# Kernel tuning notes

Measured on AMD Instinct MI355X. Metric: run time of the kernel, lower is better.

## Reference

```python
import jax, jax.numpy as jnp
import numpy as np


def setup_inputs() -> dict:
    key = jax.random.key(0)
    k0, k1, k2, k3, k4 = jax.random.split(key, 5)
    B, S, H, I, E = 4, 2048, 1024, 3584, 8
    scale = 0.02
    return {
        "hidden_states": jax.random.normal(k0, (B, S, H), jnp.float32),
        "gate_w": jax.random.normal(k1, (E, H), jnp.float32) * scale,
        "Wg": jax.random.normal(k2, (E, I, H), jnp.float32) * scale,
        "Wu": jax.random.normal(k3, (E, I, H), jnp.float32) * scale,
        "Wd": jax.random.normal(k4, (E, H, I), jnp.float32) * scale,
        "top_k": 2,
    }


def reference(hidden_states, gate_w, Wg, Wu, Wd, top_k):
    B, S, H = hidden_states.shape
    E = gate_w.shape[0]
    x = hidden_states.reshape(-1, H)  # [N, H]

    # Router: softmax in float32 (matches torch dtype=torch.float), then top-k + renorm.
    router_logits = x @ gate_w.T  # [N, E]
    routing_probs = jax.nn.softmax(router_logits.astype(jnp.float32), axis=-1)
    top_w, sel = jax.lax.top_k(routing_probs, top_k)  # [N, K]
    top_w = top_w / jnp.sum(top_w, axis=-1, keepdims=True)
    top_w = top_w.astype(x.dtype)

    # Combined per-token weight for each expert: sum of top-k weights routed to it.
    # comb[n, e] = sum_k top_w[n, k] * (sel[n, k] == e)
    comb = jnp.einsum("nk,nke->ne", top_w, jax.nn.one_hot(sel, E, dtype=x.dtype))

    out = jnp.zeros_like(x)
    for e in range(E):  # fixed small loop over experts (structurally distinct weights)
        h = jax.nn.silu(x @ Wg[e].T) * (x @ Wu[e].T)  # [N, I] SwiGLU
        out = out + (h @ Wd[e].T) * comb[:, e:e + 1]
    return out.reshape(B, S, H), router_logits
```

## Files before the change

### kernel.cpp

```cpp
#include <hip/hip_runtime.h>
#include <hip/hip_bf16.h>

#define N_TOK 8192
#define H_DIM 1024
#define I_DIM 3584
#define N_EXP 8
#define N_PAIR (N_TOK * 2)

#define BM 256
#define BN 128
#define BK 32
#define MAX_TILES 72

#define NPAN1 (I_DIM / BN)
#define NPAN2 (H_DIM / BN)
#define NWG1  (MAX_TILES * NPAN1)
#define NWG2  (MAX_TILES * NPAN2 * 2)

typedef short bf16x8 __attribute__((ext_vector_type(8)));
typedef float f32x4 __attribute__((ext_vector_type(4)));

#define CFENCE() asm volatile("" ::: "memory")


#define WS_CNT      0
#define WS_FILL     64
#define WS_OFF      128
#define WS_NTILES   192
#define WS_TILETAB  256
#define WS_SEL      2048
#define WS_WGT      (WS_SEL    + 2 * N_TOK * 4)
#define WS_PTOK     (WS_WGT    + 2 * N_TOK * 4)
#define WS_PW       (WS_PTOK   + N_PAIR * 4)
#define WS_XBF      (WS_PW     + N_PAIR * 4)
#define WS_HBUF     (WS_XBF    + (size_t)N_TOK * H_DIM * 2)
#define WBF_ELEMS   ((size_t)N_EXP * I_DIM * H_DIM)
#define WS_WGBF     (WS_HBUF + (size_t)N_PAIR * I_DIM * 2)
#define WS_WUBF     (WS_WGBF + WBF_ELEMS * 2)
#define WS_END      (WS_WUBF + WBF_ELEMS * 2)

__device__ __forceinline__ unsigned short f2bf(float f) {
  unsigned int u = __float_as_uint(f);
  unsigned int r = (u + 0x7fffu + ((u >> 16) & 1u)) >> 16;
  return (unsigned short)r;
}

__device__ __forceinline__ uint4 pack8(float4 a, float4 b) {
  uint4 r;
  r.x = (unsigned)f2bf(a.x) | ((unsigned)f2bf(a.y) << 16);
  r.y = (unsigned)f2bf(a.z) | ((unsigned)f2bf(a.w) << 16);
  r.z = (unsigned)f2bf(b.x) | ((unsigned)f2bf(b.y) << 16);
  r.w = (unsigned)f2bf(b.z) | ((unsigned)f2bf(b.w) << 16);
  return r;
}

__device__ __forceinline__ void gll16(const ushort* g, ushort* l) {
  __builtin_amdgcn_global_load_lds(
      (const __attribute__((address_space(1))) unsigned int*)g,
      (__attribute__((address_space(3))) unsigned int*)l, 16, 0, 0);
}

__global__ __launch_bounds__(64) void k_router(
    const float* __restrict__ x, const float* __restrict__ gw,
    float* __restrict__ logits, int* __restrict__ sel,
    float* __restrict__ wgt, int* __restrict__ cnt,
    ushort* __restrict__ xbf)
{
  const int n = blockIdx.x;
  const int lane = threadIdx.x;
  const float4* xr = (const float4*)(x + (size_t)n * H_DIM + lane * 16);
  float4 x0 = xr[0], x1 = xr[1], x2 = xr[2], x3 = xr[3];

  uint4* xo = (uint4*)(xbf + (size_t)n * H_DIM + lane * 16);
  xo[0] = pack8(x0, x1);
  xo[1] = pack8(x2, x3);

  float l[N_EXP];
#pragma unroll
  for (int e = 0; e < N_EXP; ++e) {
    const float4* wr = (const float4*)(gw + e * H_DIM + lane * 16);
    float4 w0 = wr[0], w1 = wr[1], w2 = wr[2], w3 = wr[3];
    float p = x0.x * w0.x + x0.y * w0.y + x0.z * w0.z + x0.w * w0.w
            + x1.x * w1.x + x1.y * w1.y + x1.z * w1.z + x1.w * w1.w
            + x2.x * w2.x + x2.y * w2.y + x2.z * w2.z + x2.w * w2.w
            + x3.x * w3.x + x3.y * w3.y + x3.z * w3.z + x3.w * w3.w;
#pragma unroll
    for (int o = 32; o >= 1; o >>= 1) p += __shfl_xor(p, o, 64);
    l[e] = p;
  }
  float m = l[0];
#pragma unroll
  for (int e = 1; e < N_EXP; ++e) m = fmaxf(m, l[e]);
  float pr[N_EXP]; float den = 0.f;
#pragma unroll
  for (int e = 0; e < N_EXP; ++e) { pr[e] = expf(l[e] - m); den += pr[e]; }
#pragma unroll
  for (int e = 0; e < N_EXP; ++e) pr[e] /= den;
  int i0 = 0; float p0 = pr[0];
#pragma unroll
  for (int e = 1; e < N_EXP; ++e) { if (pr[e] > p0) { p0 = pr[e]; i0 = e; } }
  int i1 = -1; float p1 = -1.f;
#pragma unroll
  for (int e = 0; e < N_EXP; ++e) { if (e != i0 && pr[e] > p1) { p1 = pr[e]; i1 = e; } }
  float rs = 1.f / (p0 + p1);
  if (lane == 0) {
    float* lo = logits + (size_t)n * N_EXP;
#pragma unroll
    for (int e = 0; e < N_EXP; ++e) lo[e] = l[e];
    sel[2 * n] = i0; sel[2 * n + 1] = i1;
    wgt[2 * n] = p0 * rs; wgt[2 * n + 1] = p1 * rs;
    atomicAdd(&cnt[i0], 1);
    atomicAdd(&cnt[i1], 1);
  }
}

__global__ void k_prefix(const int* __restrict__ cnt, int* __restrict__ off,
                         int* __restrict__ ntiles, int* __restrict__ tab)
{
  if (threadIdx.x != 0 || blockIdx.x != 0) return;
  int acc = 0, nt = 0;
  for (int e = 0; e < N_EXP; ++e) {
    off[e] = acc;
    int c = cnt[e];
    for (int r = 0; r < c; r += BM) {
      tab[nt * 3 + 0] = e;
      tab[nt * 3 + 1] = acc + r;
      tab[nt * 3 + 2] = (c - r < BM) ? (c - r) : BM;
      nt++;
    }
    acc += c;
  }
  off[N_EXP] = acc;
  *ntiles = nt;
}

__global__ __launch_bounds__(256) void k_scatter(
    const int* __restrict__ sel, const float* __restrict__ wgt,
    const int* __restrict__ off, int* __restrict__ fill,
    int* __restrict__ ptok, float* __restrict__ pw)
{
  int n = blockIdx.x * 256 + threadIdx.x;
  if (n >= N_TOK) return;
#pragma unroll
  for (int k = 0; k < 2; ++k) {
    int e = sel[2 * n + k];
    int pos = atomicAdd(&fill[e], 1);
    int row = off[e] + pos;
    ptok[row] = n;
    pw[row] = wgt[2 * n + k];
  }
}

__global__ __launch_bounds__(256) void k_cvtw(const float* __restrict__ src,
                                              ushort* __restrict__ dst)
{
  size_t i = (size_t)blockIdx.x * 256 + threadIdx.x;
  const float4* s = (const float4*)(src + i * 8);
  float4 a = s[0], b = s[1];
  ((uint4*)dst)[i] = pack8(a, b);
}


__global__ __launch_bounds__(512) void k_mlp1b(
    const ushort* __restrict__ Wg, const ushort* __restrict__ Wu,
    const ushort* __restrict__ xbf, const int* __restrict__ ptok,
    const int* __restrict__ ntiles, const int* __restrict__ tab,
    ushort* __restrict__ hbuf)
{
  __shared__ ushort sA[2][BM * BK];
  __shared__ ushort sG[2][BN * BK];
  __shared__ ushort sU[2][BN * BK];
  __shared__ int stok[BM];

  const int orig = blockIdx.x;
  const int lin = (orig & 7) * (NWG1 >> 3) + (orig >> 3);
  const int tile = lin / NPAN1;
  const int i0 = (lin % NPAN1) * BN;

  if (tile >= *ntiles) return;
  const int e = tab[tile * 3 + 0];
  const int row0 = tab[tile * 3 + 1];
  const int nrows = tab[tile * 3 + 2];
  const int t = threadIdx.x;

  if (t < BM) {
    int tt = t < nrows ? t : (nrows - 1);
    stok[t] = ptok[row0 + tt];
  }
  __syncthreads();

  const int ak = (((t & 3) ^ ((t >> 3) & 3)) * 8);
  const int ar = t >> 2;
  const ushort* ga0 = xbf + (size_t)stok[ar] * H_DIM + ak;
  const ushort* ga1 = xbf + (size_t)stok[128 + ar] * H_DIM + ak;

  const ushort* gg0 = Wg + (size_t)e * I_DIM * H_DIM + (size_t)(i0 + ar) * H_DIM + ak;
  const ushort* gu0 = Wu + (size_t)e * I_DIM * H_DIM + (size_t)(i0 + ar) * H_DIM + ak;

  const int lane = t & 63, wid = t >> 6;
  const int wm = wid >> 1, wn = wid & 1;
  const int fr = lane & 15, fq = lane >> 4;
  const int fs = (fq ^ ((fr >> 1) & 3)) * 8;

  f32x4 ag[4][4], au[4][4];
#pragma unroll
  for (int m = 0; m < 4; ++m)
#pragma unroll
    for (int n = 0; n < 4; ++n) { ag[m][n] = (f32x4){0,0,0,0}; au[m][n] = (f32x4){0,0,0,0}; }

#define STAGE1(b, kt) do {                      \
    gll16(ga0 + (kt), &sA[b][t * 8]);           \
    gll16(ga1 + (kt), &sA[b][(512 + t) * 8]);   \
    gll16(gg0 + (kt), &sG[b][t * 8]);           \
    gll16(gu0 + (kt), &sU[b][t * 8]);           \
  } while (0)

#define COMPUTE1(b) do {                                                     \
    bf16x8 a[4], bg[4], bu[4];                                               \
    _Pragma("unroll")                                                        \
    for (int m = 0; m < 4; ++m)                                              \
      a[m] = *(const bf16x8*)(&sA[b][(wm * 64 + m * 16 + fr) * BK + fs]);    \
    _Pragma("unroll")                                                        \
    for (int n = 0; n < 4; ++n) {                                            \
      bg[n] = *(const bf16x8*)(&sG[b][(wn * 64 + n * 16 + fr) * BK + fs]);   \
      bu[n] = *(const bf16x8*)(&sU[b][(wn * 64 + n * 16 + fr) * BK + fs]);   \
    }                                                                        \
    _Pragma("unroll")                                                        \
    for (int m = 0; m < 4; ++m)                                              \
      _Pragma("unroll")                                                      \
      for (int n = 0; n < 4; ++n) {                                          \
        ag[m][n] = __builtin_amdgcn_mfma_f32_16x16x32_bf16(a[m], bg[n], ag[m][n], 0, 0, 0); \
        au[m][n] = __builtin_amdgcn_mfma_f32_16x16x32_bf16(a[m], bu[n], au[m][n], 0, 0, 0); \
      }                                                                      \
  } while (0)

  const int NK = H_DIM / BK;
  STAGE1(0, 0);
  CFENCE();
  STAGE1(1, BK);
#pragma unroll 2
  for (int ki = 0; ki < NK - 2; ++ki) {
    const int cur = ki & 1;
    asm volatile("s_waitcnt vmcnt(4)" ::: "memory");
    __builtin_amdgcn_s_barrier();
    CFENCE();
    __builtin_amdgcn_sched_barrier(0);
    COMPUTE1(cur);
    asm volatile("s_waitcnt lgkmcnt(0)" ::: "memory");
    __builtin_amdgcn_sched_barrier(0);
    __builtin_amdgcn_s_barrier();
    CFENCE();
    STAGE1(cur, (ki + 2) * BK);
  }
  asm volatile("s_waitcnt vmcnt(4)" ::: "memory");
  __builtin_amdgcn_s_barrier();
  CFENCE();
  __builtin_amdgcn_sched_barrier(0);
  COMPUTE1(0);
  CFENCE();
  asm volatile("s_waitcnt vmcnt(0) lgkmcnt(0)" ::: "memory");
  __builtin_amdgcn_s_barrier();
  CFENCE();
  __builtin_amdgcn_sched_barrier(0);
  COMPUTE1(1);
#undef STAGE1
#undef COMPUTE1

#pragma unroll
  for (int m = 0; m < 4; ++m) {
    const int rb = wm * 64 + m * 16 + fq * 4;
#pragma unroll
    for (int n = 0; n < 4; ++n) {
      const int col = i0 + wn * 64 + n * 16 + fr;
#pragma unroll
      for (int r = 0; r < 4; ++r) {
        const int row = rb + r;
        if (row < nrows) {
          float g = ag[m][n][r], u = au[m][n][r];
          float hv = (g / (1.f + __expf(-g))) * u;
          hbuf[(size_t)(row0 + row) * I_DIM + col] = f2bf(hv);
        }
      }
    }
  }
}

__global__ __launch_bounds__(512) void k_mlp2b(
    const ushort* __restrict__ Wd, const ushort* __restrict__ hbuf,
    const int* __restrict__ ptok, const float* __restrict__ pw,
    const int* __restrict__ ntiles, const int* __restrict__ tab,
    float* __restrict__ out)
{
  __shared__ ushort sA[2][BM * BK];
  __shared__ ushort sB[2][BN * BK];
  __shared__ int stok[BM];
  __shared__ float sw[BM];

  const int orig = blockIdx.x;
  const int lin = (orig & 7) * (NWG2 >> 3) + (orig >> 3);
  const int tile = lin >> 4;
  const int rem = lin & 15;
  const int j0 = (rem >> 1) * BN;
  const int kz = rem & 1;

  if (tile >= *ntiles) return;
  const int e = tab[tile * 3 + 0];
  const int row0 = tab[tile * 3 + 1];
  const int nrows = tab[tile * 3 + 2];
  const int t = threadIdx.x;

  if (t < BM) {
    int tt = t < nrows ? t : (nrows - 1);
    stok[t] = ptok[row0 + tt];
    sw[t] = pw[row0 + tt];
  }
  __syncthreads();

  const int KHALF = I_DIM / 2;
  const int kbase = kz * KHALF;

  const int ak = (((t & 3) ^ ((t >> 3) & 3)) * 8);
  const int ar = t >> 2;
  int arow0 = row0 + ar;        if (arow0 > N_PAIR - 1) arow0 = N_PAIR - 1;
  int arow1 = row0 + 128 + ar;  if (arow1 > N_PAIR - 1) arow1 = N_PAIR - 1;
  const ushort* ga0 = hbuf + (size_t)arow0 * I_DIM + kbase + ak;
  const ushort* ga1 = hbuf + (size_t)arow1 * I_DIM + kbase + ak;

  const ushort* gb0 = Wd + (size_t)e * H_DIM * I_DIM + (size_t)(j0 + ar) * I_DIM + kbase + ak;

  const int lane = t & 63, wid = t >> 6;
  const int wm = wid >> 1, wn = wid & 1;
  const int fr = lane & 15, fq = lane >> 4;
  const int fs = (fq ^ ((fr >> 1) & 3)) * 8;

  f32x4 ac[4][4];
#pragma unroll
  for (int m = 0; m < 4; ++m)
#pragma unroll
    for (int n = 0; n < 4; ++n) ac[m][n] = (f32x4){0,0,0,0};

#define STAGE2(b, kt) do {                      \
    gll16(ga0 + (kt), &sA[b][t * 8]);           \
    gll16(ga1 + (kt), &sA[b][(512 + t) * 8]);   \
    gll16(gb0 + (kt), &sB[b][t * 8]);           \
  } while (0)

#define COMPUTE2(b) do {                                                     \
    bf16x8 a[4], bb[4];                                                      \
    _Pragma("unroll")                                                        \
    for (int m = 0; m < 4; ++m)                                              \
      a[m] = *(const bf16x8*)(&sA[b][(wm * 64 + m * 16 + fr) * BK + fs]);    \
    _Pragma("unroll")                                                        \
    for (int n = 0; n < 4; ++n)                                              \
      bb[n] = *(const bf16x8*)(&sB[b][(wn * 64 + n * 16 + fr) * BK + fs]);   \
    _Pragma("unroll")                                                        \
    for (int m = 0; m < 4; ++m)                                              \
      _Pragma("unroll")                                                      \
      for (int n = 0; n < 4; ++n)                                            \
        ac[m][n] = __builtin_amdgcn_mfma_f32_16x16x32_bf16(a[m], bb[n], ac[m][n], 0, 0, 0); \
  } while (0)

  const int NK = KHALF / BK;
  STAGE2(0, 0);
  CFENCE();
  STAGE2(1, BK);
#pragma unroll 2
  for (int ki = 0; ki < NK - 2; ++ki) {
    const int cur = ki & 1;
    asm volatile("s_waitcnt vmcnt(3)" ::: "memory");
    __builtin_amdgcn_s_barrier();
    CFENCE();
    __builtin_amdgcn_sched_barrier(0);
    COMPUTE2(cur);
    asm volatile("s_waitcnt lgkmcnt(0)" ::: "memory");
    __builtin_amdgcn_sched_barrier(0);
    __builtin_amdgcn_s_barrier();
    CFENCE();
    STAGE2(cur, (ki + 2) * BK);
  }
  asm volatile("s_waitcnt vmcnt(3)" ::: "memory");
  __builtin_amdgcn_s_barrier();
  CFENCE();
  __builtin_amdgcn_sched_barrier(0);
  COMPUTE2(0);
  CFENCE();
  asm volatile("s_waitcnt vmcnt(0) lgkmcnt(0)" ::: "memory");
  __builtin_amdgcn_s_barrier();
  CFENCE();
  __builtin_amdgcn_sched_barrier(0);
  COMPUTE2(1);
#undef STAGE2
#undef COMPUTE2

#pragma unroll
  for (int m = 0; m < 4; ++m) {
    const int rb = wm * 64 + m * 16 + fq * 4;
#pragma unroll
    for (int n = 0; n < 4; ++n) {
      const int col = j0 + wn * 64 + n * 16 + fr;
#pragma unroll
      for (int r = 0; r < 4; ++r) {
        const int row = rb + r;
        if (row < nrows) {
          float v = ac[m][n][r] * sw[row];
          atomicAdd(&out[(size_t)stok[row] * H_DIM + col], v);
        }
      }
    }
  }
}


#define FBM 128
#define FBN 128

__global__ __launch_bounds__(256) void k_mlp1(
    const float* __restrict__ Wg, const float* __restrict__ Wu,
    const ushort* __restrict__ xbf, const int* __restrict__ ptok,
    const int* __restrict__ ntiles, const int* __restrict__ tab,
    ushort* __restrict__ hbuf)
{
  __shared__ ushort sA[FBM * BK];
  __shared__ ushort sG[FBN * BK];
  __shared__ ushort sU[FBN * BK];
  __shared__ int stok[FBM];

  const int tile = blockIdx.x;
  if (tile >= *ntiles) return;
  const int e = tab[tile * 3 + 0];
  const int row0 = tab[tile * 3 + 1] + (blockIdx.z ? FBM : 0);
  int nrows = tab[tile * 3 + 2] - (blockIdx.z ? FBM : 0);
  if (nrows <= 0) return;
  if (nrows > FBM) nrows = FBM;
  const int i0 = blockIdx.y * FBN;
  const int t = threadIdx.x;

  if (t < FBM) {
    int tt = t < nrows ? t : (nrows - 1);
    stok[t] = ptok[row0 + tt];
  }
  __syncthreads();

  const int ak = (t & 3) * 8;
  const ushort* ga0 = xbf + (size_t)stok[t >> 2] * H_DIM + ak;
  const ushort* ga1 = xbf + (size_t)stok[64 + (t >> 2)] * H_DIM + ak;
  ushort* la0 = sA + (size_t)t * 8;
  ushort* la1 = sA + (size_t)(256 + t) * 8;

  const int wr = t >> 1, wcb = (t & 1) * 16;
  const float* gwg = Wg + (size_t)e * I_DIM * H_DIM + (size_t)(i0 + wr) * H_DIM + wcb;
  const float* gwu = Wu + (size_t)e * I_DIM * H_DIM + (size_t)(i0 + wr) * H_DIM + wcb;
  ushort* lwg = sG + wr * BK + wcb;
  ushort* lwu = sU + wr * BK + wcb;

  const int lane = t & 63, wid = t >> 6;
  const int wm = wid >> 1, wn = wid & 1;
  const int fr = lane & 15, fq = lane >> 4;

  f32x4 ag[4][4], au[4][4];
#pragma unroll
  for (int m = 0; m < 4; ++m)
#pragma unroll
    for (int n = 0; n < 4; ++n) { ag[m][n] = (f32x4){0,0,0,0}; au[m][n] = (f32x4){0,0,0,0}; }

  for (int kt = 0; kt < H_DIM; kt += BK) {
    gll16(ga0 + kt, la0);
    gll16(ga1 + kt, la1);

    const float4* pg = (const float4*)(gwg + kt);
    const float4* pu = (const float4*)(gwu + kt);
    float4 g0 = pg[0], g1 = pg[1], g2 = pg[2], g3 = pg[3];
    float4 u0 = pu[0], u1 = pu[1], u2 = pu[2], u3 = pu[3];
    ((uint4*)lwg)[0] = pack8(g0, g1);
    ((uint4*)lwg)[1] = pack8(g2, g3);
    ((uint4*)lwu)[0] = pack8(u0, u1);
    ((uint4*)lwu)[1] = pack8(u2, u3);
    __syncthreads();

    bf16x8 a[4], bg[4], bu[4];
#pragma unroll
    for (int m = 0; m < 4; ++m)
      a[m] = *(const bf16x8*)(sA + (wm * 64 + m * 16 + fr) * BK + fq * 8);
#pragma unroll
    for (int n = 0; n < 4; ++n) {
      bg[n] = *(const bf16x8*)(sG + (wn * 64 + n * 16 + fr) * BK + fq * 8);
      bu[n] = *(const bf16x8*)(sU + (wn * 64 + n * 16 + fr) * BK + fq * 8);
    }
#pragma unroll
    for (int m = 0; m < 4; ++m)
#pragma unroll
      for (int n = 0; n < 4; ++n) {
        ag[m][n] = __builtin_amdgcn_mfma_f32_16x16x32_bf16(a[m], bg[n], ag[m][n], 0, 0, 0);
        au[m][n] = __builtin_amdgcn_mfma_f32_16x16x32_bf16(a[m], bu[n], au[m][n], 0, 0, 0);
      }
    __syncthreads();
  }

#pragma unroll
  for (int m = 0; m < 4; ++m) {
    const int rb = wm * 64 + m * 16 + fq * 4;
#pragma unroll
    for (int n = 0; n < 4; ++n) {
      const int col = i0 + wn * 64 + n * 16 + fr;
#pragma unroll
      for (int r = 0; r < 4; ++r) {
        const int row = rb + r;
        if (row < nrows) {
          float g = ag[m][n][r], u = au[m][n][r];
          float hv = (g / (1.f + __expf(-g))) * u;
          hbuf[(size_t)(row0 + row) * I_DIM + col] = f2bf(hv);
        }
      }
    }
  }
}

__global__ __launch_bounds__(256) void k_mlp2(
    const float* __restrict__ Wd, const ushort* __restrict__ hbuf,
    const int* __restrict__ ptok, const float* __restrict__ pw,
    const int* __restrict__ ntiles, const int* __restrict__ tab,
    float* __restrict__ out)
{
  __shared__ ushort sA[FBM * BK];
  __shared__ ushort sB[FBN * BK];
  __shared__ int stok[FBM];
  __shared__ float sw[FBM];

  const int tile = blockIdx.x;
  if (tile >= *ntiles) return;
  const int e = tab[tile * 3 + 0];
  const int row0 = tab[tile * 3 + 1] + (blockIdx.z ? FBM : 0);
  int nrows = tab[tile * 3 + 2] - (blockIdx.z ? FBM : 0);
  if (nrows <= 0) return;
  if (nrows > FBM) nrows = FBM;
  const int j0 = blockIdx.y * FBN;
  const int t = threadIdx.x;

  if (t < FBM) {
    int tt = t < nrows ? t : (nrows - 1);
    stok[t] = ptok[row0 + tt];
    sw[t] = pw[row0 + tt];
  }
  __syncthreads();

  const int ak = (t & 3) * 8;
  int arow0 = row0 + (t >> 2);       if (arow0 > N_PAIR - 1) arow0 = N_PAIR - 1;
  int arow1 = row0 + 64 + (t >> 2);  if (arow1 > N_PAIR - 1) arow1 = N_PAIR - 1;
  const ushort* ga0 = hbuf + (size_t)arow0 * I_DIM + ak;
  const ushort* ga1 = hbuf + (size_t)arow1 * I_DIM + ak;
  ushort* la0 = sA + (size_t)t * 8;
  ushort* la1 = sA + (size_t)(256 + t) * 8;

  const int wr = t >> 1, wcb = (t & 1) * 16;
  const float* gb = Wd + (size_t)e * H_DIM * I_DIM + (size_t)(j0 + wr) * I_DIM + wcb;
  ushort* lb = sB + wr * BK + wcb;

  const int lane = t & 63, wid = t >> 6;
  const int wm = wid >> 1, wn = wid & 1;
  const int fr = lane & 15, fq = lane >> 4;

  f32x4 ac[4][4];
#pragma unroll
  for (int m = 0; m < 4; ++m)
#pragma unroll
    for (int n = 0; n < 4; ++n) ac[m][n] = (f32x4){0,0,0,0};

  for (int kt = 0; kt < I_DIM; kt += BK) {
    gll16(ga0 + kt, la0);
    gll16(ga1 + kt, la1);

    const float4* pb = (const float4*)(gb + kt);
    float4 b0 = pb[0], b1 = pb[1], b2 = pb[2], b3 = pb[3];
    ((uint4*)lb)[0] = pack8(b0, b1);
    ((uint4*)lb)[1] = pack8(b2, b3);
    __syncthreads();

    bf16x8 a[4], bb[4];
#pragma unroll
    for (int m = 0; m < 4; ++m)
      a[m] = *(const bf16x8*)(sA + (wm * 64 + m * 16 + fr) * BK + fq * 8);
#pragma unroll
    for (int n = 0; n < 4; ++n)
      bb[n] = *(const bf16x8*)(sB + (wn * 64 + n * 16 + fr) * BK + fq * 8);
#pragma unroll
    for (int m = 0; m < 4; ++m)
#pragma unroll
      for (int n = 0; n < 4; ++n)
        ac[m][n] = __builtin_amdgcn_mfma_f32_16x16x32_bf16(a[m], bb[n], ac[m][n], 0, 0, 0);
    __syncthreads();
  }

#pragma unroll
  for (int m = 0; m < 4; ++m) {
    const int rb = wm * 64 + m * 16 + fq * 4;
#pragma unroll
    for (int n = 0; n < 4; ++n) {
      const int col = j0 + wn * 64 + n * 16 + fr;
#pragma unroll
      for (int r = 0; r < 4; ++r) {
        const int row = rb + r;
        if (row < nrows) {
          float v = ac[m][n][r] * sw[row];
          atomicAdd(&out[(size_t)stok[row] * H_DIM + col], v);
        }
      }
    }
  }
}

extern "C" void kernel_launch(void* const* d_in, const int* in_sizes, int n_in,
                              void* d_out, int out_size, void* d_ws, size_t ws_size,
                              hipStream_t stream)
{
  const float* x  = (const float*)d_in[0];
  const float* gw = (const float*)d_in[1];
  const float* Wg = (const float*)d_in[2];
  const float* Wu = (const float*)d_in[3];
  const float* Wd = (const float*)d_in[4];

  float* out    = (float*)d_out;
  float* logits = out + (size_t)N_TOK * H_DIM;

  char* ws = (char*)d_ws;
  int*    cnt    = (int*)(ws + WS_CNT);
  int*    fill   = (int*)(ws + WS_FILL);
  int*    off    = (int*)(ws + WS_OFF);
  int*    ntiles = (int*)(ws + WS_NTILES);
  int*    tab    = (int*)(ws + WS_TILETAB);
  int*    sel    = (int*)(ws + WS_SEL);
  float*  wgt    = (float*)(ws + WS_WGT);
  int*    ptok   = (int*)(ws + WS_PTOK);
  float*  pw     = (float*)(ws + WS_PW);
  ushort* xbf    = (ushort*)(ws + WS_XBF);
  ushort* hbuf   = (ushort*)(ws + WS_HBUF);
  ushort* wgbf   = (ushort*)(ws + WS_WGBF);
  ushort* wubf   = (ushort*)(ws + WS_WUBF);
  ushort* wdbf   = wgbf;

  const bool fast = (ws_size >= WS_END);

  hipMemsetAsync(d_out, 0, (size_t)N_TOK * H_DIM * sizeof(float), stream);
  hipMemsetAsync(ws, 0, 128, stream);

  k_router<<<N_TOK, 64, 0, stream>>>(x, gw, logits, sel, wgt, cnt, xbf);
  k_prefix<<<1, 64, 0, stream>>>(cnt, off, ntiles, tab);
  k_scatter<<<N_TOK / 256, 256, 0, stream>>>(sel, wgt, off, fill, ptok, pw);

  const int cvtblocks = (int)(WBF_ELEMS / 8 / 256);

  if (fast) {
    k_cvtw<<<cvtblocks, 256, 0, stream>>>(Wg, wgbf);
    k_cvtw<<<cvtblocks, 256, 0, stream>>>(Wu, wubf);
    k_mlp1b<<<NWG1, 512, 0, stream>>>(wgbf, wubf, xbf, ptok, ntiles, tab, hbuf);
    k_cvtw<<<cvtblocks, 256, 0, stream>>>(Wd, wdbf);
    k_mlp2b<<<NWG2, 512, 0, stream>>>(wdbf, hbuf, ptok, pw, ntiles, tab, out);
  } else {
    dim3 gA(MAX_TILES, I_DIM / FBN, 2);
    dim3 gB(MAX_TILES, H_DIM / FBN, 2);
    k_mlp1<<<gA, 256, 0, stream>>>(Wg, Wu, xbf, ptok, ntiles, tab, hbuf);
    k_mlp2<<<gB, 256, 0, stream>>>(Wd, hbuf, ptok, pw, ntiles, tab, out);
  }
}
```

Baseline: 959.0 us.

## Triple-buffer MoE GEMMs, interleave loads with MFMAs, replace atomics with reduce pass

Both grouped GEMM kernels move from double to triple LDS buffering and issue the next stage's global-to-LDS loads between MFMA groups, with wave priority raised around the MFMAs. The down-projection drops its split-K over two halves and atomicAdd epilogue: when workspace allows, each pair row writes to a per-pair output buffer and a separate reduce kernel sums the two expert contributions per token. This also removes the output memset. The cost is more LDS per block, fewer down-projection workgroups, and an extra fp32 buffer written and read back.

Result: slower. 1.102 ms (+15.0%).

```diff
diff --git a/kernel.cpp b/kernel.cpp
--- a/kernel.cpp
+++ b/kernel.cpp
@@ -15,13 +15,14 @@
 #define NPAN1 (I_DIM / BN)
 #define NPAN2 (H_DIM / BN)
 #define NWG1  (MAX_TILES * NPAN1)
-#define NWG2  (MAX_TILES * NPAN2 * 2)
+#define NWG2  (MAX_TILES * NPAN2)
 
 typedef short bf16x8 __attribute__((ext_vector_type(8)));
 typedef float f32x4 __attribute__((ext_vector_type(4)));
 
 #define CFENCE() asm volatile("" ::: "memory")
 
+#define MFMA_BF16 __builtin_amdgcn_mfma_f32_16x16x32_bf16
 
 #define WS_CNT      0
 #define WS_FILL     64
@@ -38,6 +39,9 @@
 #define WS_WGBF     (WS_HBUF + (size_t)N_PAIR * I_DIM * 2)
 #define WS_WUBF     (WS_WGBF + WBF_ELEMS * 2)
 #define WS_END      (WS_WUBF + WBF_ELEMS * 2)
+#define WS_TOKROW   WS_END
+#define WS_OBUF     (WS_TOKROW + (size_t)2 * N_TOK * 4)
+#define WS_END2     (WS_OBUF + (size_t)N_PAIR * H_DIM * 4)
 
 __device__ __forceinline__ unsigned short f2bf(float f) {
   unsigned int u = __float_as_uint(f);
@@ -137,7 +141,8 @@
 __global__ __launch_bounds__(256) void k_scatter(
     const int* __restrict__ sel, const float* __restrict__ wgt,
     const int* __restrict__ off, int* __restrict__ fill,
-    int* __restrict__ ptok, float* __restrict__ pw)
+    int* __restrict__ ptok, float* __restrict__ pw,
+    int* __restrict__ tokrow)
 {
   int n = blockIdx.x * 256 + threadIdx.x;
   if (n >= N_TOK) return;
@@ -148,6 +153,7 @@
     int row = off[e] + pos;
     ptok[row] = n;
     pw[row] = wgt[2 * n + k];
+    if (tokrow) tokrow[2 * n + k] = row;
   }
 }
 
@@ -158,6 +164,21 @@
   const float4* s = (const float4*)(src + i * 8);
   float4 a = s[0], b = s[1];
   ((uint4*)dst)[i] = pack8(a, b);
+}
+
+__global__ __launch_bounds__(256) void k_reduce(
+    const float* __restrict__ obuf, const int* __restrict__ tokrow,
+    float* __restrict__ out)
+{
+  const int n = blockIdx.x;
+  const int t = threadIdx.x;
+  const int r0 = tokrow[2 * n];
+  const int r1 = tokrow[2 * n + 1];
+  const float4* p0 = (const float4*)(obuf + (size_t)r0 * H_DIM);
+  const float4* p1 = (const float4*)(obuf + (size_t)r1 * H_DIM);
+  float4 a = p0[t], b = p1[t];
+  float4 v = make_float4(a.x + b.x, a.y + b.y, a.z + b.z, a.w + b.w);
+  ((float4*)(out + (size_t)n * H_DIM))[t] = v;
 }
 
 
@@ -167,9 +188,9 @@
     const int* __restrict__ ntiles, const int* __restrict__ tab,
     ushort* __restrict__ hbuf)
 {
-  __shared__ ushort sA[2][BM * BK];
-  __shared__ ushort sG[2][BN * BK];
-  __shared__ ushort sU[2][BN * BK];
+  __shared__ ushort sA[3][BM * BK];
+  __shared__ ushort sG[3][BN * BK];
+  __shared__ ushort sU[3][BN * BK];
   __shared__ int stok[BM];
 
   const int orig = blockIdx.x;
@@ -193,7 +214,6 @@
   const int ar = t >> 2;
   const ushort* ga0 = xbf + (size_t)stok[ar] * H_DIM + ak;
   const ushort* ga1 = xbf + (size_t)stok[128 + ar] * H_DIM + ak;
-
   const ushort* gg0 = Wg + (size_t)e * I_DIM * H_DIM + (size_t)(i0 + ar) * H_DIM + ak;
   const ushort* gu0 = Wu + (size_t)e * I_DIM * H_DIM + (size_t)(i0 + ar) * H_DIM + ak;
 
@@ -215,56 +235,303 @@
     gll16(gu0 + (kt), &sU[b][t * 8]);           \
   } while (0)
 
-#define COMPUTE1(b) do {                                                     \
-    bf16x8 a[4], bg[4], bu[4];                                               \
-    _Pragma("unroll")                                                        \
-    for (int m = 0; m < 4; ++m)                                              \
-      a[m] = *(const bf16x8*)(&sA[b][(wm * 64 + m * 16 + fr) * BK + fs]);    \
-    _Pragma("unroll")                                                        \
-    for (int n = 0; n < 4; ++n) {                                            \
-      bg[n] = *(const bf16x8*)(&sG[b][(wn * 64 + n * 16 + fr) * BK + fs]);   \
-      bu[n] = *(const bf16x8*)(&sU[b][(wn * 64 + n * 16 + fr) * BK + fs]);   \
-    }                                                                        \
-    _Pragma("unroll")                                                        \
-    for (int m = 0; m < 4; ++m)                                              \
-      _Pragma("unroll")                                                      \
-      for (int n = 0; n < 4; ++n) {                                          \
-        ag[m][n] = __builtin_amdgcn_mfma_f32_16x16x32_bf16(a[m], bg[n], ag[m][n], 0, 0, 0); \
-        au[m][n] = __builtin_amdgcn_mfma_f32_16x16x32_bf16(a[m], bu[n], au[m][n], 0, 0, 0); \
-      }                                                                      \
+#define STEP1(rb, wb, KT, DOSTAGE) do {                                       \
+    bf16x8 a_[4];                                                             \
+    _Pragma("unroll")                                                         \
+    for (int m = 0; m < 4; ++m)                                               \
+      a_[m] = *(const bf16x8*)(&sA[rb][(wm * 64 + m * 16 + fr) * BK + fs]);   \
+    _Pragma("unroll")                                                         \
+    for (int n = 0; n < 4; ++n) {                                             \
+      bf16x8 bg_ = *(const bf16x8*)(&sG[rb][(wn * 64 + n * 16 + fr) * BK + fs]); \
+      bf16x8 bu_ = *(const bf16x8*)(&sU[rb][(wn * 64 + n * 16 + fr) * BK + fs]); \
+      __builtin_amdgcn_s_setprio(1);                                          \
+      _Pragma("unroll")                                                       \
+      for (int m = 0; m < 4; ++m) {                                           \
+        ag[m][n] = MFMA_BF16(a_[m], bg_, ag[m][n], 0, 0, 0);                  \
+        au[m][n] = MFMA_BF16(a_[m], bu_, au[m][n], 0, 0, 0);                  \
+      }                                                                       \
+      __builtin_amdgcn_s_setprio(0);                                          \
+      if (DOSTAGE) {                                                          \
+        if (n == 0) gll16(ga0 + (KT), &sA[wb][t * 8]);                        \
+        if (n == 1) gll16(ga1 + (KT), &sA[wb][(512 + t) * 8]);                \
+        if (n == 2) gll16(gg0 + (KT), &sG[wb][t * 8]);                        \
+        if (n == 3) gll16(gu0 + (KT), &sU[wb][t * 8]);                        \
+      }                                                                       \
+      CFENCE();                                                               \
+    }                                                                         \
   } while (0)
 
   const int NK = H_DIM / BK;
   STAGE1(0, 0);
   CFENCE();
   STAGE1(1, BK);
-#pragma unroll 2
-  for (int ki = 0; ki < NK - 2; ++ki) {
-    const int cur = ki & 1;
+  CFENCE();
+
+  int rb = 0;
+  for (int ki = 0; ki <= NK - 3; ++ki) {
     asm volatile("s_waitcnt vmcnt(4)" ::: "memory");
     __builtin_amdgcn_s_barrier();
     CFENCE();
     __builtin_amdgcn_sched_barrier(0);
-    COMPUTE1(cur);
+    const int wb = (rb + 2 >= 3) ? rb - 1 : rb + 2;
+    STEP1(rb, wb, (ki + 2) * BK, 1);
     asm volatile("s_waitcnt lgkmcnt(0)" ::: "memory");
     __builtin_amdgcn_sched_barrier(0);
     __builtin_amdgcn_s_barrier();
     CFENCE();
-    STAGE1(cur, (ki + 2) * BK);
+    rb = (rb + 1 >= 3) ? 0 : rb + 1;
   }
   asm volatile("s_waitcnt vmcnt(4)" ::: "memory");
   __builtin_amdgcn_s_barrier();
   CFENCE();
   __builtin_amdgcn_sched_barrier(0);
-  COMPUTE1(0);
-  CFENCE();
-  asm volatile("s_waitcnt vmcnt(0) lgkmcnt(0)" ::: "memory");
+  STEP1(rb, 0, 0, 0);
+  rb = (rb + 1 >= 3) ? 0 : rb + 1;
+  asm volatile("s_waitcnt vmcnt(0)" ::: "memory");
   __builtin_amdgcn_s_barrier();
   CFENCE();
   __builtin_amdgcn_sched_barrier(0);
-  COMPUTE1(1);
+  STEP1(rb, 0, 0, 0);
+#undef STEP1
 #undef STAGE1
-#undef COMPUTE1
+
+#pragma unroll
+  for (int m = 0; m < 4; ++m) {
+    const int rbv = wm * 64 + m * 16 + fq * 4;
+#pragma unroll
+    for (int n = 0; n < 4; ++n) {
+      const int col = i0 + wn * 64 + n * 16 + fr;
+#pragma unroll
+      for (int r = 0; r < 4; ++r) {
+        const int row = rbv + r;
+        if (row < nrows) {
+          float g = ag[m][n][r], u = au[m][n][r];
+          float hv = (g / (1.f + __expf(-g))) * u;
+          hbuf[(size_t)(row0 + row) * I_DIM + col] = f2bf(hv);
+        }
+      }
+    }
+  }
+}
+
+template <int EPI>
+__global__ __launch_bounds__(512) void k_mlp2b(
+    const ushort* __restrict__ Wd, const ushort* __restrict__ hbuf,
+    const int* __restrict__ ptok, const float* __restrict__ pw,
+    const int* __restrict__ ntiles, const int* __restrict__ tab,
+    float* __restrict__ dst)
+{
+  __shared__ ushort sA[3][BM * BK];
+  __shared__ ushort sB[3][BN * BK];
+  __shared__ int stok[BM];
+  __shared__ float sw[BM];
+
+  const int orig = blockIdx.x;
+  const int lin = (orig & 7) * (NWG2 >> 3) + (orig >> 3);
+  const int tile = lin / NPAN2;
+  const int j0 = (lin % NPAN2) * BN;
+
+  if (tile >= *ntiles) return;
+  const int e = tab[tile * 3 + 0];
+  const int row0 = tab[tile * 3 + 1];
+  const int nrows = tab[tile * 3 + 2];
+  const int t = threadIdx.x;
+
+  if (t < BM) {
+    int tt = t < nrows ? t : (nrows - 1);
+    stok[t] = ptok[row0 + tt];
+    sw[t] = pw[row0 + tt];
+  }
+  __syncthreads();
+
+  const int ak = (((t & 3) ^ ((t >> 3) & 3)) * 8);
+  const int ar = t >> 2;
+  int arow0 = row0 + ar;        if (arow0 > N_PAIR - 1) arow0 = N_PAIR - 1;
+  int arow1 = row0 + 128 + ar;  if (arow1 > N_PAIR - 1) arow1 = N_PAIR - 1;
+  const ushort* ga0 = hbuf + (size_t)arow0 * I_DIM + ak;
+  const ushort* ga1 = hbuf + (size_t)arow1 * I_DIM + ak;
+  const ushort* gb0 = Wd + (size_t)e * H_DIM * I_DIM + (size_t)(j0 + ar) * I_DIM + ak;
+
+  const int lane = t & 63, wid = t >> 6;
+  const int wm = wid >> 1, wn = wid & 1;
+  const int fr = lane & 15, fq = lane >> 4;
+  const int fs = (fq ^ ((fr >> 1) & 3)) * 8;
+
+  f32x4 ac[4][4];
+#pragma unroll
+  for (int m = 0; m < 4; ++m)
+#pragma unroll
+    for (int n = 0; n < 4; ++n) ac[m][n] = (f32x4){0,0,0,0};
+
+#define STAGE2(b, kt) do {                      \
+    gll16(ga0 + (kt), &sA[b][t * 8]);           \
+    gll16(ga1 + (kt), &sA[b][(512 + t) * 8]);   \
+    gll16(gb0 + (kt), &sB[b][t * 8]);           \
+  } while (0)
+
+#define STEP2(rb, wb, KT, DOSTAGE) do {                                       \
+    bf16x8 a_[4];                                                             \
+    _Pragma("unroll")                                                         \
+    for (int m = 0; m < 4; ++m)                                               \
+      a_[m] = *(const bf16x8*)(&sA[rb][(wm * 64 + m * 16 + fr) * BK + fs]);   \
+    _Pragma("unroll")                                                         \
+    for (int n = 0; n < 4; ++n) {                                             \
+      bf16x8 bb_ = *(const bf16x8*)(&sB[rb][(wn * 64 + n * 16 + fr) * BK + fs]); \
+      __builtin_amdgcn_s_setprio(1);                                          \
+      _Pragma("unroll")                                                       \
+      for (int m = 0; m < 4; ++m)                                             \
+        ac[m][n] = MFMA_BF16(a_[m], bb_, ac[m][n], 0, 0, 0);                  \
+      __builtin_amdgcn_s_setprio(0);                                          \
+      if (DOSTAGE) {                                                          \
+        if (n == 0) gll16(ga0 + (KT), &sA[wb][t * 8]);                        \
+        if (n == 1) gll16(ga1 + (KT), &sA[wb][(512 + t) * 8]);                \
+        if (n == 2) gll16(gb0 + (KT), &sB[wb][t * 8]);                        \
+      }                                                                       \
+      CFENCE();                                                               \
+    }                                                                         \
+  } while (0)
+
+  const int NK = I_DIM / BK;
+  STAGE2(0, 0);
+  CFENCE();
+  STAGE2(1, BK);
+  CFENCE();
+
+  int rb = 0;
+  for (int ki = 0; ki <= NK - 3; ++ki) {
+    asm volatile("s_waitcnt vmcnt(3)" ::: "memory");
+    __builtin_amdgcn_s_barrier();
+    CFENCE();
+    __builtin_amdgcn_sched_barrier(0);
+    const int wb = (rb + 2 >= 3) ? rb - 1 : rb + 2;
+    STEP2(rb, wb, (ki + 2) * BK, 1);
+    asm volatile("s_waitcnt lgkmcnt(0)" ::: "memory");
+    __builtin_amdgcn_sched_barrier(0);
+    __builtin_amdgcn_s_barrier();
+    CFENCE();
+    rb = (rb + 1 >= 3) ? 0 : rb + 1;
+  }
+  asm volatile("s_waitcnt vmcnt(3)" ::: "memory");
+  __builtin_amdgcn_s_barrier();
+  CFENCE();
+  __builtin_amdgcn_sched_barrier(0);
+  STEP2(rb, 0, 0, 0);
+  rb = (rb + 1 >= 3) ? 0 : rb + 1;
+  asm volatile("s_waitcnt vmcnt(0)" ::: "memory");
+  __builtin_amdgcn_s_barrier();
+  CFENCE();
+  __builtin_amdgcn_sched_barrier(0);
+  STEP2(rb, 0, 0, 0);
+#undef STEP2
+#undef STAGE2
+
+#pragma unroll
+  for (int m = 0; m < 4; ++m) {
+    const int rbv = wm * 64 + m * 16 + fq * 4;
+#pragma unroll
+    for (int n = 0; n < 4; ++n) {
+      const int col = j0 + wn * 64 + n * 16 + fr;
+#pragma unroll
+      for (int r = 0; r < 4; ++r) {
+        const int row = rbv + r;
+        if (row < nrows) {
+          float v = ac[m][n][r] * sw[row];
+          if (EPI == 0) {
+            dst[(size_t)(row0 + row) * H_DIM + col] = v;
+          } else {
+            atomicAdd(&dst[(size_t)stok[row] * H_DIM + col], v);
+          }
+        }
+      }
+    }
+  }
+}
+
+
+#define FBM 128
+#define FBN 128
+
+__global__ __launch_bounds__(256) void k_mlp1(
+    const float* __restrict__ Wg, const float* __restrict__ Wu,
+    const ushort* __restrict__ xbf, const int* __restrict__ ptok,
+    const int* __restrict__ ntiles, const int* __restrict__ tab,
+    ushort* __restrict__ hbuf)
+{
+  __shared__ ushort sA[FBM * BK];
+  __shared__ ushort sG[FBN * BK];
+  __shared__ ushort sU[FBN * BK];
+  __shared__ int stok[FBM];
+
+  const int tile = blockIdx.x;
+  if (tile >= *ntiles) return;
+  const int e = tab[tile * 3 + 0];
+  const int row0 = tab[tile * 3 + 1] + (blockIdx.z ? FBM : 0);
+  int nrows = tab[tile * 3 + 2] - (blockIdx.z ? FBM : 0);
+  if (nrows <= 0) return;
+  if (nrows > FBM) nrows = FBM;
+  const int i0 = blockIdx.y * FBN;
+  const int t = threadIdx.x;
+
+  if (t < FBM) {
+    int tt = t < nrows ? t : (nrows - 1);
+    stok[t] = ptok[row0 + tt];
+  }
+  __syncthreads();
+
+  const int ak = (t & 3) * 8;
+  const ushort* ga0 = xbf + (size_t)stok[t >> 2] * H_DIM + ak;
+  const ushort* ga1 = xbf + (size_t)stok[64 + (t >> 2)] * H_DIM + ak;
+  ushort* la0 = sA + (size_t)t * 8;
+  ushort* la1 = sA + (size_t)(256 + t) * 8;
+
+  const int wr = t >> 1, wcb = (t & 1) * 16;
+  const float* gwg = Wg + (size_t)e * I_DIM * H_DIM + (size_t)(i0 + wr) * H_DIM + wcb;
+  const float* gwu = Wu + (size_t)e * I_DIM * H_DIM + (size_t)(i0 + wr) * H_DIM + wcb;
+  ushort* lwg = sG + wr * BK + wcb;
+  ushort* lwu = sU + wr * BK + wcb;
+
+  const int lane = t & 63, wid = t >> 6;
+  const int wm = wid >> 1, wn = wid & 1;
+  const int fr = lane & 15, fq = lane >> 4;
+
+  f32x4 ag[4][4], au[4][4];
+#pragma unroll
+  for (int m = 0; m < 4; ++m)
+#pragma unroll
+    for (int n = 0; n < 4; ++n) { ag[m][n] = (f32x4){0,0,0,0}; au[m][n] = (f32x4){0,0,0,0}; }
+
+  for (int kt = 0; kt < H_DIM; kt += BK) {
+    gll16(ga0 + kt, la0);
+    gll16(ga1 + kt, la1);
+
+    const float4* pg = (const float4*)(gwg + kt);
+    const float4* pu = (const float4*)(gwu + kt);
+    float4 g0 = pg[0], g1 = pg[1], g2 = pg[2], g3 = pg[3];
+    float4 u0 = pu[0], u1 = pu[1], u2 = pu[2], u3 = pu[3];
+    ((uint4*)lwg)[0] = pack8(g0, g1);
+    ((uint4*)lwg)[1] = pack8(g2, g3);
+    ((uint4*)lwu)[0] = pack8(u0, u1);
+    ((uint4*)lwu)[1] = pack8(u2, u3);
+    __syncthreads();
+
+    bf16x8 a[4], bg[4], bu[4];
+#pragma unroll
+    for (int m = 0; m < 4; ++m)
+      a[m] = *(const bf16x8*)(sA + (wm * 64 + m * 16 + fr) * BK + fq * 8);
+#pragma unroll
+    for (int n = 0; n < 4; ++n) {
+      bg[n] = *(const bf16x8*)(sG + (wn * 64 + n * 16 + fr) * BK + fq * 8);
+      bu[n] = *(const bf16x8*)(sU + (wn * 64 + n * 16 + fr) * BK + fq * 8);
+    }
+#pragma unroll
+    for (int m = 0; m < 4; ++m)
+#pragma unroll
+      for (int n = 0; n < 4; ++n) {
+        ag[m][n] = MFMA_BF16(a[m], bg[n], ag[m][n], 0, 0, 0);
+        au[m][n] = MFMA_BF16(a[m], bu[n], au[m][n], 0, 0, 0);
+      }
+    __syncthreads();
+  }
 
 #pragma unroll
   for (int m = 0; m < 4; ++m) {
@@ -285,236 +552,6 @@
   }
 }
 
-__global__ __launch_bounds__(512) void k_mlp2b(
-    const ushort* __restrict__ Wd, const ushort* __restrict__ hbuf,
-    const int* __restrict__ ptok, const float* __restrict__ pw,
-    const int* __restrict__ ntiles, const int* __restrict__ tab,
-    float* __restrict__ out)
-{
-  __shared__ ushort sA[2][BM * BK];
-  __shared__ ushort sB[2][BN * BK];
-  __shared__ int stok[BM];
-  __shared__ float sw[BM];
-
-  const int orig = blockIdx.x;
-  const int lin = (orig & 7) * (NWG2 >> 3) + (orig >> 3);
-  const int tile = lin >> 4;
-  const int rem = lin & 15;
-  const int j0 = (rem >> 1) * BN;
-  const int kz = rem & 1;
-
-  if (tile >= *ntiles) return;
-  const int e = tab[tile * 3 + 0];
-  const int row0 = tab[tile * 3 + 1];
-  const int nrows = tab[tile * 3 + 2];
-  const int t = threadIdx.x;
-
-  if (t < BM) {
-    int tt = t < nrows ? t : (nrows - 1);
-    stok[t] = ptok[row0 + tt];
-    sw[t] = pw[row0 + tt];
-  }
-  __syncthreads();
-
-  const int KHALF = I_DIM / 2;
-  const int kbase = kz * KHALF;
-
-  const int ak = (((t & 3) ^ ((t >> 3) & 3)) * 8);
-  const int ar = t >> 2;
-  int arow0 = row0 + ar;        if (arow0 > N_PAIR - 1) arow0 = N_PAIR - 1;
-  int arow1 = row0 + 128 + ar;  if (arow1 > N_PAIR - 1) arow1 = N_PAIR - 1;
-  const ushort* ga0 = hbuf + (size_t)arow0 * I_DIM + kbase + ak;
-  const ushort* ga1 = hbuf + (size_t)arow1 * I_DIM + kbase + ak;
-
-  const ushort* gb0 = Wd + (size_t)e * H_DIM * I_DIM + (size_t)(j0 + ar) * I_DIM + kbase + ak;
-
-  const int lane = t & 63, wid = t >> 6;
-  const int wm = wid >> 1, wn = wid & 1;
-  const int fr = lane & 15, fq = lane >> 4;
-  const int fs = (fq ^ ((fr >> 1) & 3)) * 8;
-
-  f32x4 ac[4][4];
-#pragma unroll
-  for (int m = 0; m < 4; ++m)
-#pragma unroll
-    for (int n = 0; n < 4; ++n) ac[m][n] = (f32x4){0,0,0,0};
-
-#define STAGE2(b, kt) do {                      \
-    gll16(ga0 + (kt), &sA[b][t * 8]);           \
-    gll16(ga1 + (kt), &sA[b][(512 + t) * 8]);   \
-    gll16(gb0 + (kt), &sB[b][t * 8]);           \
-  } while (0)
-
-#define COMPUTE2(b) do {                                                     \
-    bf16x8 a[4], bb[4];                                                      \
-    _Pragma("unroll")                                                        \
-    for (int m = 0; m < 4; ++m)                                              \
-      a[m] = *(const bf16x8*)(&sA[b][(wm * 64 + m * 16 + fr) * BK + fs]);    \
-    _Pragma("unroll")                                                        \
-    for (int n = 0; n < 4; ++n)                                              \
-      bb[n] = *(const bf16x8*)(&sB[b][(wn * 64 + n * 16 + fr) * BK + fs]);   \
-    _Pragma("unroll")                                                        \
-    for (int m = 0; m < 4; ++m)                                              \
-      _Pragma("unroll")                                                      \
-      for (int n = 0; n < 4; ++n)                                            \
-        ac[m][n] = __builtin_amdgcn_mfma_f32_16x16x32_bf16(a[m], bb[n], ac[m][n], 0, 0, 0); \
-  } while (0)
-
-  const int NK = KHALF / BK;
-  STAGE2(0, 0);
-  CFENCE();
-  STAGE2(1, BK);
-#pragma unroll 2
-  for (int ki = 0; ki < NK - 2; ++ki) {
-    const int cur = ki & 1;
-    asm volatile("s_waitcnt vmcnt(3)" ::: "memory");
-    __builtin_amdgcn_s_barrier();
-    CFENCE();
-    __builtin_amdgcn_sched_barrier(0);
-    COMPUTE2(cur);
-    asm volatile("s_waitcnt lgkmcnt(0)" ::: "memory");
-    __builtin_amdgcn_sched_barrier(0);
-    __builtin_amdgcn_s_barrier();
-    CFENCE();
-    STAGE2(cur, (ki + 2) * BK);
-  }
-  asm volatile("s_waitcnt vmcnt(3)" ::: "memory");
-  __builtin_amdgcn_s_barrier();
-  CFENCE();
-  __builtin_amdgcn_sched_barrier(0);
-  COMPUTE2(0);
-  CFENCE();
-  asm volatile("s_waitcnt vmcnt(0) lgkmcnt(0)" ::: "memory");
-  __builtin_amdgcn_s_barrier();
-  CFENCE();
-  __builtin_amdgcn_sched_barrier(0);
-  COMPUTE2(1);
-#undef STAGE2
-#undef COMPUTE2
-
-#pragma unroll
-  for (int m = 0; m < 4; ++m) {
-    const int rb = wm * 64 + m * 16 + fq * 4;
-#pragma unroll
-    for (int n = 0; n < 4; ++n) {
-      const int col = j0 + wn * 64 + n * 16 + fr;
-#pragma unroll
-      for (int r = 0; r < 4; ++r) {
-        const int row = rb + r;
-        if (row < nrows) {
-          float v = ac[m][n][r] * sw[row];
-          atomicAdd(&out[(size_t)stok[row] * H_DIM + col], v);
-        }
-      }
-    }
-  }
-}
-
-
-#define FBM 128
-#define FBN 128
-
-__global__ __launch_bounds__(256) void k_mlp1(
-    const float* __restrict__ Wg, const float* __restrict__ Wu,
-    const ushort* __restrict__ xbf, const int* __restrict__ ptok,
-    const int* __restrict__ ntiles, const int* __restrict__ tab,
-    ushort* __restrict__ hbuf)
-{
-  __shared__ ushort sA[FBM * BK];
-  __shared__ ushort sG[FBN * BK];
-  __shared__ ushort sU[FBN * BK];
-  __shared__ int stok[FBM];
-
-  const int tile = blockIdx.x;
-  if (tile >= *ntiles) return;
-  const int e = tab[tile * 3 + 0];
-  const int row0 = tab[tile * 3 + 1] + (blockIdx.z ? FBM : 0);
-  int nrows = tab[tile * 3 + 2] - (blockIdx.z ? FBM : 0);
-  if (nrows <= 0) return;
-  if (nrows > FBM) nrows = FBM;
-  const int i0 = blockIdx.y * FBN;
-  const int t = threadIdx.x;
-
-  if (t < FBM) {
-    int tt = t < nrows ? t : (nrows - 1);
-    stok[t] = ptok[row0 + tt];
-  }
-  __syncthreads();
-
-  const int ak = (t & 3) * 8;
-  const ushort* ga0 = xbf + (size_t)stok[t >> 2] * H_DIM + ak;
-  const ushort* ga1 = xbf + (size_t)stok[64 + (t >> 2)] * H_DIM + ak;
-  ushort* la0 = sA + (size_t)t * 8;
-  ushort* la1 = sA + (size_t)(256 + t) * 8;
-
-  const int wr = t >> 1, wcb = (t & 1) * 16;
-  const float* gwg = Wg + (size_t)e * I_DIM * H_DIM + (size_t)(i0 + wr) * H_DIM + wcb;
-  const float* gwu = Wu + (size_t)e * I_DIM * H_DIM + (size_t)(i0 + wr) * H_DIM + wcb;
-  ushort* lwg = sG + wr * BK + wcb;
-  ushort* lwu = sU + wr * BK + wcb;
-
-  const int lane = t & 63, wid = t >> 6;
-  const int wm = wid >> 1, wn = wid & 1;
-  const int fr = lane & 15, fq = lane >> 4;
-
-  f32x4 ag[4][4], au[4][4];
-#pragma unroll
-  for (int m = 0; m < 4; ++m)
-#pragma unroll
-    for (int n = 0; n < 4; ++n) { ag[m][n] = (f32x4){0,0,0,0}; au[m][n] = (f32x4){0,0,0,0}; }
-
-  for (int kt = 0; kt < H_DIM; kt += BK) {
-    gll16(ga0 + kt, la0);
-    gll16(ga1 + kt, la1);
-
-    const float4* pg = (const float4*)(gwg + kt);
-    const float4* pu = (const float4*)(gwu + kt);
-    float4 g0 = pg[0], g1 = pg[1], g2 = pg[2], g3 = pg[3];
-    float4 u0 = pu[0], u1 = pu[1], u2 = pu[2], u3 = pu[3];
-    ((uint4*)lwg)[0] = pack8(g0, g1);
-    ((uint4*)lwg)[1] = pack8(g2, g3);
-    ((uint4*)lwu)[0] = pack8(u0, u1);
-    ((uint4*)lwu)[1] = pack8(u2, u3);
-    __syncthreads();
-
-    bf16x8 a[4], bg[4], bu[4];
-#pragma unroll
-    for (int m = 0; m < 4; ++m)
-      a[m] = *(const bf16x8*)(sA + (wm * 64 + m * 16 + fr) * BK + fq * 8);
-#pragma unroll
-    for (int n = 0; n < 4; ++n) {
-      bg[n] = *(const bf16x8*)(sG + (wn * 64 + n * 16 + fr) * BK + fq * 8);
-      bu[n] = *(const bf16x8*)(sU + (wn * 64 + n * 16 + fr) * BK + fq * 8);
-    }
-#pragma unroll
-    for (int m = 0; m < 4; ++m)
-#pragma unroll
-      for (int n = 0; n < 4; ++n) {
-        ag[m][n] = __builtin_amdgcn_mfma_f32_16x16x32_bf16(a[m], bg[n], ag[m][n], 0, 0, 0);
-        au[m][n] = __builtin_amdgcn_mfma_f32_16x16x32_bf16(a[m], bu[n], au[m][n], 0, 0, 0);
-      }
-    __syncthreads();
-  }
-
-#pragma unroll
-  for (int m = 0; m < 4; ++m) {
-    const int rb = wm * 64 + m * 16 + fq * 4;
-#pragma unroll
-    for (int n = 0; n < 4; ++n) {
-      const int col = i0 + wn * 64 + n * 16 + fr;
-#pragma unroll
-      for (int r = 0; r < 4; ++r) {
-        const int row = rb + r;
-        if (row < nrows) {
-          float g = ag[m][n][r], u = au[m][n][r];
-          float hv = (g / (1.f + __expf(-g))) * u;
-          hbuf[(size_t)(row0 + row) * I_DIM + col] = f2bf(hv);
-        }
-      }
-    }
-  }
-}
-
 __global__ __launch_bounds__(256) void k_mlp2(
     const float* __restrict__ Wd, const ushort* __restrict__ hbuf,
     const int* __restrict__ ptok, const float* __restrict__ pw,
@@ -586,7 +623,7 @@
     for (int m = 0; m < 4; ++m)
 #pragma unroll
       for (int n = 0; n < 4; ++n)
-        ac[m][n] = __builtin_amdgcn_mfma_f32_16x16x32_bf16(a[m], bb[n], ac[m][n], 0, 0, 0);
+        ac[m][n] = MFMA_BF16(a[m], bb[n], ac[m][n], 0, 0, 0);
     __syncthreads();
   }
 
@@ -636,15 +673,19 @@
   ushort* wgbf   = (ushort*)(ws + WS_WGBF);
   ushort* wubf   = (ushort*)(ws + WS_WUBF);
   ushort* wdbf   = wgbf;
-
-  const bool fast = (ws_size >= WS_END);
-
-  hipMemsetAsync(d_out, 0, (size_t)N_TOK * H_DIM * sizeof(float), stream);
+  int*    tokrow = (int*)(ws + WS_TOKROW);
+  float*  obuf   = (float*)(ws + WS_OBUF);
+
+  const bool fast  = (ws_size >= WS_END);
+  const bool fast2 = (ws_size >= WS_END2);
+
+  if (!fast2) hipMemsetAsync(d_out, 0, (size_t)N_TOK * H_DIM * sizeof(float), stream);
   hipMemsetAsync(ws, 0, 128, stream);
 
   k_router<<<N_TOK, 64, 0, stream>>>(x, gw, logits, sel, wgt, cnt, xbf);
   k_prefix<<<1, 64, 0, stream>>>(cnt, off, ntiles, tab);
-  k_scatter<<<N_TOK / 256, 256, 0, stream>>>(sel, wgt, off, fill, ptok, pw);
+  k_scatter<<<N_TOK / 256, 256, 0, stream>>>(sel, wgt, off, fill, ptok, pw,
+                                             fast2 ? tokrow : (int*)nullptr);
 
   const int cvtblocks = (int)(WBF_ELEMS / 8 / 256);
 
@@ -653,7 +694,12 @@
     k_cvtw<<<cvtblocks, 256, 0, stream>>>(Wu, wubf);
     k_mlp1b<<<NWG1, 512, 0, stream>>>(wgbf, wubf, xbf, ptok, ntiles, tab, hbuf);
     k_cvtw<<<cvtblocks, 256, 0, stream>>>(Wd, wdbf);
-    k_mlp2b<<<NWG2, 512, 0, stream>>>(wdbf, hbuf, ptok, pw, ntiles, tab, out);
+    if (fast2) {
+      k_mlp2b<0><<<NWG2, 512, 0, stream>>>(wdbf, hbuf, ptok, pw, ntiles, tab, obuf);
+      k_reduce<<<N_TOK, 256, 0, stream>>>(obuf, tokrow, out);
+    } else {
+      k_mlp2b<1><<<NWG2, 512, 0, stream>>>(wdbf, hbuf, ptok, pw, ntiles, tab, out);
+    }
   } else {
     dim3 gA(MAX_TILES, I_DIM / FBN, 2);
     dim3 gB(MAX_TILES, H_DIM / FBN, 2);
```
